# Performance work log

Hardware: AMD Instinct MI355X
Metric: run time of the kernel (lower is better)

The kernel has to match this reference:

```python
import jax, jax.numpy as jnp
import numpy as np

N_NODES = 10000
N_EDGES = 640000
D_FEAT = 128
D_OUT = 128


def setup_inputs() -> dict:
    key = jax.random.key(0)
    ks = jax.random.split(key, 7)
    feat = jax.random.normal(ks[0], (N_NODES, D_FEAT), dtype=jnp.float32)
    # src_fc: Linear(D_FEAT, D_FEAT); fc: Linear(2*D_FEAT, D_OUT). torch Linear weight is [out, in].
    W_src = jax.random.normal(ks[1], (D_FEAT, D_FEAT), dtype=jnp.float32) * (1.0 / np.sqrt(D_FEAT))
    b_src = jax.random.normal(ks[2], (D_FEAT,), dtype=jnp.float32) * 0.01
    W_fc = jax.random.normal(ks[3], (D_OUT, 2 * D_FEAT), dtype=jnp.float32) * (1.0 / np.sqrt(2 * D_FEAT))
    b_fc = jax.random.normal(ks[4], (D_OUT,), dtype=jnp.float32) * 0.01
    src = jax.random.randint(ks[5], (N_EDGES,), 0, N_NODES, dtype=jnp.int32)
    dst = jax.random.randint(ks[6], (N_EDGES,), 0, N_NODES, dtype=jnp.int32)
    return {"feat": feat, "W_src": W_src, "b_src": b_src, "W_fc": W_fc, "b_fc": b_fc,
            "src": src, "dst": dst}


def reference(feat, W_src, b_src, W_fc, b_fc, src, dst):
    """SAGEConv forward (eval mode: dropout = identity, activation = identity).

    message: m_e = src_fc(feat[src_e])                 # [E, D]
    reduce:  neigh_v = mean_{e: dst_e = v} m_e         # [N, D]
    apply:   h_v = fc(concat(feat_v, neigh_v))         # [N, D_out]
    """
    n = feat.shape[0]
    # gather src features and apply per-edge linear transform
    m = feat[src] @ W_src.T + b_src                                  # [E, D]
    # segment mean over destination nodes (nodes with no in-edges get 0,
    # matching DGL's zero-initialized dstdata)
    agg = jax.ops.segment_sum(m, dst, num_segments=n)                # [N, D]
    deg = jax.ops.segment_sum(jnp.ones(dst.shape, feat.dtype), dst, num_segments=n)
    neigh = agg / jnp.maximum(deg, 1.0)[:, None]                     # [N, D]
    h = jnp.concatenate([feat, neigh], axis=-1) @ W_fc.T + b_fc      # [N, D_out]
    return h
```

## Files before the change

kernel.cpp:

```cpp
#include <hip/hip_runtime.h>

#define NN 10000
#define DF 128
#define NE 640000
#define GBN 16
#define NBUCK 625
#define TILE 8192
#define NTILES ((NE + TILE - 1) / TILE)
#define EPT 8
#define GCAP 2048

#define PACK_BLKS 157
#define PREP_BLKS 16

typedef __attribute__((ext_vector_type(8))) short bf16x8;
typedef __attribute__((ext_vector_type(4))) float f32x4;
typedef unsigned long long ull;

__device__ __forceinline__ unsigned int f2bf(float f) {
    unsigned int u = __float_as_uint(f);
    u = (u + 0x7FFFu + ((u >> 16) & 1u)) >> 16;
    return u;
}
__device__ __forceinline__ unsigned int pack2bf(float a, float b) {
    return f2bf(a) | (f2bf(b) << 16);
}
__device__ __forceinline__ float bf_lo(unsigned int v) { return __uint_as_float(v << 16); }
__device__ __forceinline__ float bf_hi(unsigned int v) { return __uint_as_float(v & 0xFFFF0000u); }

__global__ __launch_bounds__(1024) void prologue(const float* __restrict__ feat,
                                                 unsigned int* __restrict__ A_bf,
                                                 const int* __restrict__ dstv,
                                                 int* __restrict__ tbl,
                                                 const float* __restrict__ Wfc,
                                                 const float* __restrict__ Wsrc,
                                                 const float* __restrict__ bsrc,
                                                 unsigned int* __restrict__ Bw,
                                                 float* __restrict__ bsrc2)
{
    const int bx = blockIdx.x, tid = threadIdx.x;

    if (bx < PACK_BLKS) {
        const int id = bx * 1024 + tid;
        if (id < NN * 16) {
            const int row = id >> 4, j4 = id & 15;
            const float4 fa = *(const float4*)(feat + (size_t)row * DF + 8 * j4);
            const float4 fb = *(const float4*)(feat + (size_t)row * DF + 8 * j4 + 4);
            uint4 v;
            v.x = pack2bf(fa.x, fa.y); v.y = pack2bf(fa.z, fa.w);
            v.z = pack2bf(fb.x, fb.y); v.w = pack2bf(fb.z, fb.w);
            *(uint4*)(A_bf + (size_t)row * 64 + 4 * j4) = v;
        }
        return;
    }
    if (bx < PACK_BLKS + NTILES) {
        __shared__ int h[NBUCK];
        const int t = bx - PACK_BLKS;
        if (tid < NBUCK) h[tid] = 0;
        __syncthreads();
        const int e0 = t * TILE;
#pragma unroll
        for (int j = 0; j < EPT; ++j) {
            const int e = e0 + j * 1024 + tid;
            if (e < NE) atomicAdd(&h[dstv[e] >> 4], 1);
        }
        __syncthreads();
        if (tid < NBUCK) tbl[t * NBUCK + tid] = h[tid];
        return;
    }
    {
        __shared__ float wp[8][128];
        __shared__ float red[16];
        const int g = tid >> 7;
        const int k = tid & 127;
        const int o = (bx - PACK_BLKS - NTILES) * 8 + g;
        const float* w2 = Wfc + (size_t)o * 256 + 128;
        float acc = 0.f;
#pragma unroll 8
        for (int j = 0; j < 128; ++j)
            acc = fmaf(w2[j], Wsrc[j * 128 + k], acc);
        wp[g][k] = acc;

        float p = w2[k] * bsrc[k];
#pragma unroll
        for (int d = 32; d > 0; d >>= 1) p += __shfl_down(p, d);
        if ((tid & 63) == 0) red[tid >> 6] = p;
        __syncthreads();
        if (k < 64) {
            const float2 wf = *(const float2*)(Wfc + (size_t)o * 256 + 2 * k);
            Bw[(size_t)o * 128 + k] = pack2bf(wf.x, wf.y);
            Bw[(size_t)o * 128 + 64 + k] = pack2bf(wp[g][2 * k], wp[g][2 * k + 1]);
        }
        if (k == 0) bsrc2[o] = red[2 * g] + red[2 * g + 1];
    }
}

__global__ __launch_bounds__(1024) void bin2(const int* __restrict__ srcv,
                                             const int* __restrict__ dstv,
                                             const int* __restrict__ tbl,
                                             unsigned int* __restrict__ ents,
                                             int* __restrict__ off_g)
{
    __shared__ unsigned int ent[TILE];
    __shared__ ull wpart[16];
    __shared__ int lbase[NBUCK];
    __shared__ int lcur[NBUCK];
    __shared__ int gbase[NBUCK];

    const int tid = threadIdx.x;
    const int lane = tid & 63, wid = tid >> 6;
    const int bx = blockIdx.x;
    const int e0 = bx * TILE;
    const int n = min(TILE, NE - e0);

    int myd[EPT], mys[EPT];
#pragma unroll
    for (int j = 0; j < EPT; ++j) {
        const int e = e0 + j * 1024 + tid;
        if (e < NE) { myd[j] = dstv[e]; mys[j] = srcv[e]; }
        else { myd[j] = -1; mys[j] = 0; }
    }

    int pre = 0, tot = 0, myh = 0;
    if (tid < NBUCK) {
        for (int t = 0; t < NTILES; ++t) {
            const int c = tbl[t * NBUCK + tid];
            pre += (t < bx) ? c : 0;
            myh += (t == bx) ? c : 0;
            tot += c;
        }
    }
    const ull v = (tid < NBUCK) ? (((ull)(unsigned)tot << 32) | (unsigned)myh) : 0ull;
    ull inc = v;
#pragma unroll
    for (int d = 1; d < 64; d <<= 1) {
        const ull x = (ull)__shfl_up((unsigned long long)inc, d);
        if (lane >= d) inc += x;
    }
    if (lane == 63) wpart[wid] = inc;
    __syncthreads();
    ull wsum = 0;
    for (int w = 0; w < wid; ++w) wsum += wpart[w];
    const ull ex = wsum + inc - v;
    if (tid < NBUCK) {
        const int offb = (int)(ex >> 32);
        lbase[tid] = (int)(ex & 0xFFFFFFFFull);
        gbase[tid] = offb + pre;
        lcur[tid] = 0;
        if (bx == 0) {
            off_g[tid] = offb;
            if (tid == NBUCK - 1) off_g[NBUCK] = (int)((ex + v) >> 32);
        }
    }
    __syncthreads();

#pragma unroll
    for (int j = 0; j < EPT; ++j) {
        if (myd[j] >= 0) {
            const int b = myd[j] >> 4;
            const int p = atomicAdd(&lcur[b], 1);
            ent[lbase[b] + p] = ((unsigned)myd[j] << 14) | (unsigned)mys[j];
        }
    }
    __syncthreads();

    for (int i = tid; i < n; i += 1024) {
        const unsigned u = ent[i];
        const int b = (int)(u >> 18);
        ents[gbase[b] + (i - lbase[b])] = u;
    }
}

__global__ __launch_bounds__(512) void gather_apply(const unsigned int* __restrict__ A_bf,
                                                    const unsigned int* __restrict__ Bw,
                                                    const unsigned int* __restrict__ ents,
                                                    const int* __restrict__ off,
                                                    const float* __restrict__ bfc,
                                                    const float* __restrict__ bsrc2,
                                                    float* __restrict__ out)
{
    __shared__ unsigned int raw[GCAP];
    __shared__ unsigned short sorted[GCAP];
    __shared__ int h[GBN], base[GBN], cur[GBN];
    __shared__ unsigned int ntile[GBN][68];

    const int tid = threadIdx.x;
    const int b = blockIdx.x;
    const int rbase = b * GBN;
    const int r0 = off[b], r1 = off[b + 1];
    const int cnt = min(r1 - r0, GCAP);

    if (tid < GBN) { h[tid] = 0; cur[tid] = 0; }
    __syncthreads();
    for (int i = tid; i < cnt; i += 512) {
        const unsigned u = ents[r0 + i];
        raw[i] = u;
        atomicAdd(&h[(u >> 14) & (GBN - 1)], 1);
    }
    __syncthreads();
    if (tid == 0) {
        int s = 0;
#pragma unroll
        for (int j = 0; j < GBN; ++j) { base[j] = s; s += h[j]; }
    }
    __syncthreads();
    for (int i = tid; i < cnt; i += 512) {
        const unsigned u = raw[i];
        const int dl = (int)((u >> 14) & (GBN - 1));
        const int p = base[dl] + atomicAdd(&cur[dl], 1);
        sorted[p] = (unsigned short)(u & 0x3FFFu);
    }
    __syncthreads();

    const int wave = tid >> 6, lane = tid & 63;
#pragma unroll
    for (int j = 0; j < 2; ++j) {
        const int dl = wave * 2 + j;
        const int s0 = base[dl], n = h[dl];
        float ax = 0.f, ay = 0.f;
        int i = 0;
        for (; i + 8 <= n; i += 8) {
            unsigned w[8];
#pragma unroll
            for (int q = 0; q < 8; ++q)
                w[q] = A_bf[(size_t)sorted[s0 + i + q] * 64 + lane];
#pragma unroll
            for (int q = 0; q < 8; ++q) { ax += bf_lo(w[q]); ay += bf_hi(w[q]); }
        }
        for (; i < n; ++i) {
            const unsigned a = A_bf[(size_t)sorted[s0 + i] * 64 + lane];
            ax += bf_lo(a); ay += bf_hi(a);
        }
        const float inv = (n > 0) ? 1.f / (float)n : 0.f;
        ntile[dl][lane] = pack2bf(ax * inv, ay * inv);
    }
    __syncthreads();

    const int r = lane & 15, kg = lane >> 4;

    const unsigned int* ap = A_bf + (size_t)(rbase + r) * 64 + kg * 4;
    bf16x8 a[8];
#pragma unroll
    for (int s = 0; s < 4; ++s) a[s] = *(const bf16x8*)(ap + s * 16);
#pragma unroll
    for (int s = 0; s < 4; ++s) a[4 + s] = *(const bf16x8*)(&ntile[r][s * 16 + kg * 4]);

    bool hd[4];
#pragma unroll
    for (int q = 0; q < 4; ++q) hd[q] = h[kg * 4 + q] > 0;

    const int cbase = wave * 16;
    const unsigned int* bp = Bw + (size_t)(cbase + r) * 128 + kg * 4;
    bf16x8 bb[8];
#pragma unroll
    for (int s = 0; s < 8; ++s) bb[s] = *(const bf16x8*)(bp + s * 16);
    f32x4 acc = {0.f, 0.f, 0.f, 0.f};
#pragma unroll
    for (int s = 0; s < 8; ++s)
        acc = __builtin_amdgcn_mfma_f32_16x16x32_bf16(a[s], bb[s], acc, 0, 0, 0);

    const int col = cbase + r;
    const float bc = bfc[col], bs = bsrc2[col];
#pragma unroll
    for (int q = 0; q < 4; ++q) {
        const int row = rbase + kg * 4 + q;
        out[(size_t)row * DF + col] = acc[q] + bc + (hd[q] ? bs : 0.f);
    }
}

extern "C" void kernel_launch(void* const* d_in, const int* in_sizes, int n_in,
                              void* d_out, int out_size, void* d_ws, size_t ws_size,
                              hipStream_t stream) {
    const float* feat  = (const float*)d_in[0];
    const float* W_src = (const float*)d_in[1];
    const float* b_src = (const float*)d_in[2];
    const float* W_fc  = (const float*)d_in[3];
    const float* b_fc  = (const float*)d_in[4];
    const int*   src   = (const int*)d_in[5];
    const int*   dst   = (const int*)d_in[6];
    float* out = (float*)d_out;

    unsigned int* A_bf = (unsigned int*)d_ws;
    unsigned int* Bw = A_bf + (size_t)NN * 64;
    float* bsrc2 = (float*)(Bw + 128 * 128);
    int*   off   = (int*)(bsrc2 + 128);
    int*   tbl   = off + (NBUCK + 1);
    unsigned int* ents = (unsigned int*)(tbl + (size_t)NTILES * NBUCK);

    prologue    <<<PACK_BLKS + NTILES + PREP_BLKS, 1024, 0, stream>>>(
                    feat, A_bf, dst, tbl, W_fc, W_src, b_src, Bw, bsrc2);
    bin2        <<<NTILES, 1024, 0, stream>>>(src, dst, tbl, ents, off);
    gather_apply<<<NBUCK, 512, 0, stream>>>(A_bf, Bw, ents, off, b_fc, bsrc2, out);
}
```

Baseline: 53.18 us.

## Vectorize edge index loads and gather 4 rows per wave with 16B loads

```diff
diff --git a/kernel.cpp b/kernel.cpp
--- a/kernel.cpp
+++ b/kernel.cpp
@@ -7,7 +7,6 @@
 #define NBUCK 625
 #define TILE 8192
 #define NTILES ((NE + TILE - 1) / TILE)
-#define EPT 8
 #define GCAP 2048
 
 #define PACK_BLKS 157
@@ -59,10 +58,17 @@
         if (tid < NBUCK) h[tid] = 0;
         __syncthreads();
         const int e0 = t * TILE;
-#pragma unroll
-        for (int j = 0; j < EPT; ++j) {
-            const int e = e0 + j * 1024 + tid;
-            if (e < NE) atomicAdd(&h[dstv[e] >> 4], 1);
+        const int n = min(TILE, NE - e0);
+#pragma unroll
+        for (int j = 0; j < 2; ++j) {
+            const int eb = 4 * (tid + j * 1024);
+            if (eb < n) {
+                const int4 dd = *(const int4*)(dstv + e0 + eb);
+                atomicAdd(&h[dd.x >> 4], 1);
+                atomicAdd(&h[dd.y >> 4], 1);
+                atomicAdd(&h[dd.z >> 4], 1);
+                atomicAdd(&h[dd.w >> 4], 1);
+            }
         }
         __syncthreads();
         if (tid < NBUCK) tbl[t * NBUCK + tid] = h[tid];
@@ -113,16 +119,24 @@
     const int e0 = bx * TILE;
     const int n = min(TILE, NE - e0);
 
-    int myd[EPT], mys[EPT];
-#pragma unroll
-    for (int j = 0; j < EPT; ++j) {
-        const int e = e0 + j * 1024 + tid;
-        if (e < NE) { myd[j] = dstv[e]; mys[j] = srcv[e]; }
-        else { myd[j] = -1; mys[j] = 0; }
+    int myd[8], mys[8];
+#pragma unroll
+    for (int j = 0; j < 2; ++j) {
+        const int eb = 4 * (tid + j * 1024);
+        if (eb < n) {
+            const int4 dd = *(const int4*)(dstv + e0 + eb);
+            const int4 ss = *(const int4*)(srcv + e0 + eb);
+            myd[4*j+0] = dd.x; myd[4*j+1] = dd.y; myd[4*j+2] = dd.z; myd[4*j+3] = dd.w;
+            mys[4*j+0] = ss.x; mys[4*j+1] = ss.y; mys[4*j+2] = ss.z; mys[4*j+3] = ss.w;
+        } else {
+#pragma unroll
+            for (int q = 0; q < 4; ++q) { myd[4*j+q] = -1; mys[4*j+q] = 0; }
+        }
     }
 
     int pre = 0, tot = 0, myh = 0;
     if (tid < NBUCK) {
+#pragma unroll 8
         for (int t = 0; t < NTILES; ++t) {
             const int c = tbl[t * NBUCK + tid];
             pre += (t < bx) ? c : 0;
@@ -155,7 +169,7 @@
     __syncthreads();
 
 #pragma unroll
-    for (int j = 0; j < EPT; ++j) {
+    for (int j = 0; j < 8; ++j) {
         if (myd[j] >= 0) {
             const int b = myd[j] >> 4;
             const int p = atomicAdd(&lcur[b], 1);
@@ -213,26 +227,47 @@
     __syncthreads();
 
     const int wave = tid >> 6, lane = tid & 63;
+    const int slot = lane >> 4, fl = lane & 15;
 #pragma unroll
     for (int j = 0; j < 2; ++j) {
         const int dl = wave * 2 + j;
         const int s0 = base[dl], n = h[dl];
-        float ax = 0.f, ay = 0.f;
+        float s[8] = {0.f, 0.f, 0.f, 0.f, 0.f, 0.f, 0.f, 0.f};
         int i = 0;
         for (; i + 8 <= n; i += 8) {
-            unsigned w[8];
-#pragma unroll
-            for (int q = 0; q < 8; ++q)
-                w[q] = A_bf[(size_t)sorted[s0 + i + q] * 64 + lane];
-#pragma unroll
-            for (int q = 0; q < 8; ++q) { ax += bf_lo(w[q]); ay += bf_hi(w[q]); }
-        }
-        for (; i < n; ++i) {
-            const unsigned a = A_bf[(size_t)sorted[s0 + i] * 64 + lane];
-            ax += bf_lo(a); ay += bf_hi(a);
-        }
-        const float inv = (n > 0) ? 1.f / (float)n : 0.f;
-        ntile[dl][lane] = pack2bf(ax * inv, ay * inv);
+            const int ra = sorted[s0 + i + slot];
+            const int rb = sorted[s0 + i + 4 + slot];
+            const uint4 va = *(const uint4*)(A_bf + (size_t)ra * 64 + fl * 4);
+            const uint4 vb = *(const uint4*)(A_bf + (size_t)rb * 64 + fl * 4);
+            s[0] += bf_lo(va.x) + bf_lo(vb.x); s[1] += bf_hi(va.x) + bf_hi(vb.x);
+            s[2] += bf_lo(va.y) + bf_lo(vb.y); s[3] += bf_hi(va.y) + bf_hi(vb.y);
+            s[4] += bf_lo(va.z) + bf_lo(vb.z); s[5] += bf_hi(va.z) + bf_hi(vb.z);
+            s[6] += bf_lo(va.w) + bf_lo(vb.w); s[7] += bf_hi(va.w) + bf_hi(vb.w);
+        }
+        for (; i < n; i += 4) {
+            if (i + slot < n) {
+                const int ra = sorted[s0 + i + slot];
+                const uint4 va = *(const uint4*)(A_bf + (size_t)ra * 64 + fl * 4);
+                s[0] += bf_lo(va.x); s[1] += bf_hi(va.x);
+                s[2] += bf_lo(va.y); s[3] += bf_hi(va.y);
+                s[4] += bf_lo(va.z); s[5] += bf_hi(va.z);
+                s[6] += bf_lo(va.w); s[7] += bf_hi(va.w);
+            }
+        }
+#pragma unroll
+        for (int q = 0; q < 8; ++q) {
+            s[q] += __shfl_xor(s[q], 16);
+            s[q] += __shfl_xor(s[q], 32);
+        }
+        if (slot == 0) {
+            const float inv = (n > 0) ? 1.f / (float)n : 0.f;
+            uint4 o;
+            o.x = pack2bf(s[0] * inv, s[1] * inv);
+            o.y = pack2bf(s[2] * inv, s[3] * inv);
+            o.z = pack2bf(s[4] * inv, s[5] * inv);
+            o.w = pack2bf(s[6] * inv, s[7] * inv);
+            *(uint4*)(&ntile[dl][fl * 4]) = o;
+        }
     }
     __syncthreads();
 
```

New measurement: 50.25 us (median of 2 runs). 5.5% less time.
